# Optimization experiments

Hardware: AMD Instinct MI355X
Metric: run time of the kernel (lower is better)

Reference implementation:

```python
import jax, jax.numpy as jnp
import numpy as np

C = 128
K = 7
RED = 4
C_RED = C // RED
PAD = (K - 1) // 2
BN_EPS = 1e-5


def setup_inputs() -> dict:
    key = jax.random.key(0)
    ks = jax.random.split(key, 7)
    b, h, w = 8, 56, 56
    x = jax.random.normal(ks[0], (b, C, h, w), dtype=jnp.float32)
    # 1x1 conv #1: c -> c_red
    w1 = jax.random.normal(ks[1], (C_RED, C), dtype=jnp.float32) * (1.0 / np.sqrt(C))
    b1 = jax.random.normal(ks[2], (C_RED,), dtype=jnp.float32) * 0.01
    # BatchNorm affine params
    gamma = jnp.ones((C_RED,), dtype=jnp.float32)
    beta = jnp.zeros((C_RED,), dtype=jnp.float32)
    # 1x1 conv #2: c_red -> k*k
    w2 = jax.random.normal(ks[3], (K * K, C_RED), dtype=jnp.float32) * (1.0 / np.sqrt(C_RED))
    b2 = jax.random.normal(ks[4], (K * K,), dtype=jnp.float32) * 0.01
    return {"x": x, "w1": w1, "b1": b1, "gamma": gamma, "beta": beta, "w2": w2, "b2": b2}


def _unfold(x):
    # torch.nn.Unfold(K, padding=PAD, stride=1) -> (b, c, k*k, h, w), channel-major
    b, c, h, w = x.shape
    xp = jnp.pad(x, ((0, 0), (0, 0), (PAD, PAD), (PAD, PAD)))
    patches = [xp[:, :, i:i + h, j:j + w] for i in range(K) for j in range(K)]
    return jnp.stack(patches, axis=2)  # (b, c, k*k, h, w)


def reference(x, w1, b1, gamma, beta, w2, b2):
    b, c, h, w = x.shape
    # kernel-generation branch: 1x1 conv -> BN (batch stats, training mode) -> ReLU -> 1x1 conv
    t = jnp.einsum('rc,bchw->brhw', w1, x) + b1[None, :, None, None]
    mean = t.mean(axis=(0, 2, 3))
    var = t.var(axis=(0, 2, 3))  # biased, as in torch BN normalization
    t = (t - mean[None, :, None, None]) * jax.lax.rsqrt(var + BN_EPS)[None, :, None, None]
    t = jax.nn.relu(t * gamma[None, :, None, None] + beta[None, :, None, None])
    kern = jnp.einsum('kr,brhw->bkhw', w2, t) + b2[None, :, None, None]  # (b, k*k, h, w)
    # involution: per-pixel kernel broadcast over channels, sum over k*k taps
    x_unf = _unfold(x)  # (b, c, k*k, h, w)
    return jnp.einsum('bkhw,bckhw->bchw', kern, x_unf)
```

## Files before the change

### kernel.cpp

```cpp
#include <hip/hip_runtime.h>

#define C 128
#define CRED 32
#define K 7
#define KK 49
#define H 56
#define W 56
#define P (H*W)
#define B 8
#define NPIX (B*P)
#define BN_EPS 1e-5

#define T_OFF 0
#define T_SIZE (B*CRED*P)
#define KERN_OFF (T_OFF + T_SIZE)
#define KERN_SIZE (B*KK*P)
#define NBLK_A (49*B)
#define PSUM_OFF (KERN_OFF + KERN_SIZE)
#define PSQ_OFF (PSUM_OFF + NBLK_A*CRED)
#define SS_OFF  (PSQ_OFF + NBLK_A*CRED)
#define SCALE_OFF SS_OFF
#define SHIFT_OFF (SS_OFF + CRED)
#define WS_NEED ((size_t)(SHIFT_OFF + CRED) * sizeof(float))

#define FB_SCALE_OFF T_SIZE
#define FB_SHIFT_OFF (T_SIZE + CRED)

__global__ __launch_bounds__(256) void kA_conv1(const float* __restrict__ x,
                                                const float* __restrict__ w1,
                                                const float* __restrict__ b1,
                                                float* __restrict__ ws) {
    int tid = threadIdx.x;
    int bx = blockIdx.x;
    int b  = blockIdx.y;
    int px = tid & 63;
    int p  = bx * 64 + px;
    int ru8 = __builtin_amdgcn_readfirstlane((tid >> 6) * 8);
    const float* __restrict__ wq = w1 + (size_t)ru8 * C;
    const float* xb = x + (size_t)b * C * P + p;

    float acc[8];
#pragma unroll
    for (int u = 0; u < 8; ++u) acc[u] = 0.f;
#pragma unroll 8
    for (int c = 0; c < C; ++c) {
        float xv = xb[(size_t)c * P];
#pragma unroll
        for (int u = 0; u < 8; ++u)
            acc[u] = fmaf(wq[u * C + c], xv, acc[u]);
    }
#pragma unroll
    for (int u = 0; u < 8; ++u) acc[u] += b1[ru8 + u];

    float* tb = ws + T_OFF + (size_t)b * CRED * P + p;
#pragma unroll
    for (int u = 0; u < 8; ++u)
        tb[(size_t)(ru8 + u) * P] = acc[u];

    float s[8], q[8];
#pragma unroll
    for (int u = 0; u < 8; ++u) { s[u] = acc[u]; q[u] = acc[u] * acc[u]; }
#pragma unroll
    for (int off = 32; off; off >>= 1) {
#pragma unroll
        for (int u = 0; u < 8; ++u) {
            s[u] += __shfl_xor(s[u], off);
            q[u] += __shfl_xor(q[u], off);
        }
    }
    if (px == 0) {
        int blk = b * 49 + bx;
        float* psum = ws + PSUM_OFF + (size_t)blk * CRED + ru8;
        float* psq  = ws + PSQ_OFF  + (size_t)blk * CRED + ru8;
#pragma unroll
        for (int u = 0; u < 8; ++u) { psum[u] = s[u]; psq[u] = q[u]; }
    }
}

__global__ __launch_bounds__(256) void kCB_kern(const float* __restrict__ w2,
                                                const float* __restrict__ b2,
                                                const float* __restrict__ gamma,
                                                const float* __restrict__ beta,
                                                float* __restrict__ ws) {
    __shared__ float s_t[CRED * W];
    __shared__ float s_w2[KK * 33];
    __shared__ double sd1[8][CRED];
    __shared__ double sd2[8][CRED];
    __shared__ float s_sc[CRED];
    __shared__ float s_sh[CRED];
    int tid = threadIdx.x;
    int h = blockIdx.x, b = blockIdx.y;

    {
        int r = tid & 31, seg = tid >> 5;
        double s1 = 0.0, s2 = 0.0;
        for (int i = seg * 49; i < seg * 49 + 49; ++i) {
            s1 += (double)ws[PSUM_OFF + i * CRED + r];
            s2 += (double)ws[PSQ_OFF + i * CRED + r];
        }
        sd1[seg][r] = s1; sd2[seg][r] = s2;
    }
    for (int i = tid; i < KK * CRED; i += 256) {
        int k = i >> 5, r = i & 31;
        s_w2[k * 33 + r] = w2[i];
    }
    for (int i = tid; i < CRED * W; i += 256) {
        int r = i / W, w = i - r * W;
        s_t[i] = ws[T_OFF + ((size_t)b * CRED + r) * P + h * W + w];
    }
    __syncthreads();
    if (tid < CRED) {
        double S1 = 0.0, S2 = 0.0;
        for (int g = 0; g < 8; ++g) { S1 += sd1[g][tid]; S2 += sd2[g][tid]; }
        double mean = S1 / NPIX;
        double var = S2 / NPIX - mean * mean;
        double sc = (double)gamma[tid] / sqrt(var + BN_EPS);
        s_sc[tid] = (float)sc;
        s_sh[tid] = (float)((double)beta[tid] - mean * sc);
    }
    __syncthreads();
    for (int i = tid; i < CRED * W; i += 256) {
        int r = i / W;
        s_t[i] = fmaxf(fmaf(s_t[i], s_sc[r], s_sh[r]), 0.f);
    }
    __syncthreads();
    for (int i = tid; i < KK * 14; i += 256) {
        int k = i / 14, w0 = (i - k * 14) * 4;
        float bb = b2[k];
        float a0 = bb, a1 = bb, a2 = bb, a3 = bb;
#pragma unroll
        for (int r = 0; r < CRED; ++r) {
            float4 tv = *(const float4*)&s_t[r * W + w0];
            float wv = s_w2[k * 33 + r];
            a0 = fmaf(wv, tv.x, a0);
            a1 = fmaf(wv, tv.y, a1);
            a2 = fmaf(wv, tv.z, a2);
            a3 = fmaf(wv, tv.w, a3);
        }
        float4 o = {a0, a1, a2, a3};
        *(float4*)&ws[KERN_OFF + ((size_t)b * KK + k) * P + h * W + w0] = o;
    }
}

#define TH 7
#define XROWS 13
#define XPITCH 68
__global__ __launch_bounds__(448) void kD_inv(const float* __restrict__ x,
                                              const float* __restrict__ ws,
                                              float* __restrict__ out) {
    __shared__ float4 s_x[2][XROWS * XPITCH];
    int tid = threadIdx.x;
    int bx = blockIdx.x;
    int z  = blockIdx.y;
    int b = bx >> 3, ht = bx & 7;
    int h0 = ht * TH;
    int orow = tid / W;
    int ocol = tid - orow * W;
    int sbase = orow * XPITCH + ocol;
    bool owns = orow < TH;

    int q0 = tid, q1 = tid + 448;
    int row0 = q0 >> 6, col0 = q0 & 63;
    int hh0 = h0 - 3 + row0, ww0 = col0 - 3;
    float m0 = ((unsigned)hh0 < H && (unsigned)ww0 < W) ? 1.f : 0.f;
    int off0 = (m0 != 0.f) ? (hh0 * W + ww0) : 0;
    int slot0 = row0 * XPITCH + col0;
    int row1 = q1 >> 6, col1 = q1 & 63;
    int hh1 = h0 - 3 + row1, ww1 = col1 - 3;
    bool in1 = q1 < XROWS * 64;
    float m1 = (in1 && (unsigned)hh1 < H && (unsigned)ww1 < W) ? 1.f : 0.f;
    int off1 = (m1 != 0.f) ? (hh1 * W + ww1) : 0;
    int slot1 = row1 * XPITCH + col1;

    int cg0 = z * 16;
    const size_t xbase = ((size_t)b * C + cg0) * P;

    const float* xc0 = x + xbase;
    float4 f0, f1;
    f0.x = xc0[off0] * m0;          f0.y = xc0[P + off0] * m0;
    f0.z = xc0[2 * P + off0] * m0;  f0.w = xc0[3 * P + off0] * m0;
    f1.x = xc0[off1] * m1;          f1.y = xc0[P + off1] * m1;
    f1.z = xc0[2 * P + off1] * m1;  f1.w = xc0[3 * P + off1] * m1;

    float kr[KK];
    {
        int kidx = h0 * W + tid;
        if (kidx > P - 1) kidx = P - 1;
        const float* kb = ws + KERN_OFF + (size_t)b * KK * P + kidx;
#pragma unroll
        for (int k = 0; k < KK; ++k) kr[k] = kb[(size_t)k * P];
    }

    s_x[0][slot0] = f0;
    if (in1) s_x[0][slot1] = f1;

    for (int it = 0; it < 4; ++it) {
        __syncthreads();
        float4 n0, n1;
        if (it < 3) {
            const float* xc = x + xbase + (size_t)(it + 1) * 4 * P;
            n0.x = xc[off0] * m0;          n0.y = xc[P + off0] * m0;
            n0.z = xc[2 * P + off0] * m0;  n0.w = xc[3 * P + off0] * m0;
            n1.x = xc[off1] * m1;          n1.y = xc[P + off1] * m1;
            n1.z = xc[2 * P + off1] * m1;  n1.w = xc[3 * P + off1] * m1;
        }
        if (owns) {
            const float4* xs = s_x[it & 1] + sbase;
            float a0 = 0.f, a1 = 0.f, a2 = 0.f, a3 = 0.f;
#pragma unroll
            for (int i = 0; i < K; ++i) {
#pragma unroll
                for (int j = 0; j < K; ++j) {
                    float4 xv = xs[i * XPITCH + j];
                    float kv = kr[i * 7 + j];
                    a0 = fmaf(kv, xv.x, a0);
                    a1 = fmaf(kv, xv.y, a1);
                    a2 = fmaf(kv, xv.z, a2);
                    a3 = fmaf(kv, xv.w, a3);
                }
            }
            float* ob = out + xbase + (size_t)it * 4 * P + (size_t)h0 * W + tid;
            ob[0]     = a0;
            ob[P]     = a1;
            ob[2 * P] = a2;
            ob[3 * P] = a3;
        }
        if (it < 3) {
            float4* nb = s_x[(it + 1) & 1];
            nb[slot0] = n0;
            if (in1) nb[slot1] = n1;
        }
    }
}

__global__ __launch_bounds__(256) void k1_conv1(const float* __restrict__ x,
                                                const float* __restrict__ w1,
                                                const float* __restrict__ b1,
                                                float* __restrict__ t) {
    __shared__ float s_w1t[C * CRED];
    int tid = threadIdx.x;
    for (int i = tid; i < C * CRED; i += 256) {
        int c = i >> 5, r = i & 31;
        s_w1t[i] = w1[r * C + c];
    }
    __syncthreads();
    int b = blockIdx.y;
    int p = blockIdx.x * 256 + tid;
    if (p >= P) return;
    float acc[CRED];
#pragma unroll
    for (int r = 0; r < CRED; ++r) acc[r] = 0.f;
    const float* xb = x + (size_t)b * C * P + p;
    for (int c = 0; c < C; ++c) {
        float xv = xb[(size_t)c * P];
#pragma unroll
        for (int r = 0; r < CRED; ++r)
            acc[r] = fmaf(s_w1t[c * CRED + r], xv, acc[r]);
    }
    float* tb = t + (size_t)b * CRED * P + p;
#pragma unroll
    for (int r = 0; r < CRED; ++r)
        tb[(size_t)r * P] = acc[r] + b1[r];
}

__global__ __launch_bounds__(256) void k2_bnstats(const float* __restrict__ t,
                                                  const float* __restrict__ gamma,
                                                  const float* __restrict__ beta,
                                                  float* __restrict__ scale,
                                                  float* __restrict__ shift) {
    int r = blockIdx.x;
    int tid = threadIdx.x;
    double s = 0.0, s2 = 0.0;
    for (int i = tid; i < NPIX; i += 256) {
        int b = i / P, p = i - b * P;
        float v = t[((size_t)b * CRED + r) * P + p];
        s += v;
        s2 += (double)v * v;
    }
    __shared__ double ls[256], ls2[256];
    ls[tid] = s; ls2[tid] = s2;
    __syncthreads();
    for (int off = 128; off > 0; off >>= 1) {
        if (tid < off) { ls[tid] += ls[tid + off]; ls2[tid] += ls2[tid + off]; }
        __syncthreads();
    }
    if (tid == 0) {
        double mean = ls[0] / NPIX;
        double var = ls2[0] / NPIX - mean * mean;
        double sc = (double)gamma[r] / sqrt(var + BN_EPS);
        scale[r] = (float)sc;
        shift[r] = (float)((double)beta[r] - mean * sc);
    }
}

__global__ __launch_bounds__(256) void k3_involution(const float* __restrict__ x,
                                                     const float* __restrict__ t,
                                                     const float* __restrict__ scale,
                                                     const float* __restrict__ shift,
                                                     const float* __restrict__ w2,
                                                     const float* __restrict__ b2,
                                                     float* __restrict__ out) {
    int h = blockIdx.x;
    int b = blockIdx.y;
    int z = blockIdx.z;
    int tid = threadIdx.x;
    __shared__ float s_w2[KK * CRED];
    __shared__ float s_t[CRED * W];
    __shared__ float s_kern[KK][W];
    __shared__ float s_x[4][K][64];
    for (int i = tid; i < KK * CRED; i += 256) s_w2[i] = w2[i];
    for (int i = tid; i < CRED * W; i += 256) {
        int r = i / W, w = i - r * W;
        float v = t[((size_t)b * CRED + r) * P + h * W + w];
        v = fmaf(v, scale[r], shift[r]);
        s_t[r * W + w] = fmaxf(v, 0.f);
    }
    __syncthreads();
    for (int i = tid; i < KK * W; i += 256) {
        int k = i / W, w = i - k * W;
        float acc = b2[k];
#pragma unroll
        for (int r = 0; r < CRED; ++r)
            acc = fmaf(s_w2[k * CRED + r], s_t[r * W + w], acc);
        s_kern[k][w] = acc;
    }
    __syncthreads();
    int w = tid % W;
    int c4 = tid / W;
    float kr[KK];
#pragma unroll
    for (int k = 0; k < KK; ++k) kr[k] = s_kern[k][w];
    int cbase = z * (C / 2);
    for (int cg = cbase; cg < cbase + C / 2; cg += 4) {
        for (int i = tid; i < 4 * K * 64; i += 256) {
            int col = i & 63;
            int rc = i >> 6;
            int cc = rc / K;
            int row = rc - cc * K;
            int hh = h - 3 + row;
            int ww = col - 3;
            float v = 0.f;
            if ((unsigned)hh < H && (unsigned)ww < W)
                v = x[(((size_t)b * C + cg + cc) * H + hh) * W + ww];
            s_x[cc][row][col] = v;
        }
        __syncthreads();
        if (tid < 4 * W) {
            float acc = 0.f;
#pragma unroll
            for (int i = 0; i < K; ++i)
#pragma unroll
                for (int j = 0; j < K; ++j)
                    acc = fmaf(kr[i * K + j], s_x[c4][i][w + j], acc);
            out[(((size_t)b * C + cg + c4) * H + h) * W + w] = acc;
        }
        __syncthreads();
    }
}

extern "C" void kernel_launch(void* const* d_in, const int* in_sizes, int n_in,
                              void* d_out, int out_size, void* d_ws, size_t ws_size,
                              hipStream_t stream) {
    const float* x     = (const float*)d_in[0];
    const float* w1    = (const float*)d_in[1];
    const float* b1    = (const float*)d_in[2];
    const float* gamma = (const float*)d_in[3];
    const float* beta  = (const float*)d_in[4];
    const float* w2    = (const float*)d_in[5];
    const float* b2    = (const float*)d_in[6];
    float* out = (float*)d_out;
    float* ws  = (float*)d_ws;

    if (ws_size >= WS_NEED) {
        dim3 gA(49, B);
        kA_conv1<<<gA, 256, 0, stream>>>(x, w1, b1, ws);
        dim3 gC(H, B);
        kCB_kern<<<gC, 256, 0, stream>>>(w2, b2, gamma, beta, ws);
        dim3 gD(64, 8);
        kD_inv<<<gD, 448, 0, stream>>>(x, ws, out);
    } else {
        float* t     = ws;
        float* scale = ws + FB_SCALE_OFF;
        float* shift = ws + FB_SHIFT_OFF;
        dim3 g1((P + 255) / 256, B);
        k1_conv1<<<g1, 256, 0, stream>>>(x, w1, b1, t);
        k2_bnstats<<<CRED, 256, 0, stream>>>(t, gamma, beta, scale, shift);
        dim3 g3(H, B, 2);
        k3_involution<<<g3, 256, 0, stream>>>(x, t, scale, shift, w2, b2, out);
    }
}
```

Baseline: 48.46 us.

## Fuse BN-finalize and kernel-generation conv into the involution kernel

Drops the separate kernel-generation launch. The involution kernel now reduces the BN partial stats, applies BN+ReLU to its pixel's 32 reduced channels and computes the 49 taps in registers. This removes the round trip of the per-pixel kernel tensor through global memory and one launch. To pay for the recomputation, each block now covers 32 channels instead of 16, which halves the grid to 256 blocks and could hurt occupancy. The per-thread register arrays (32 + 49 floats) add register pressure.

```diff
diff --git a/kernel.cpp b/kernel.cpp
--- a/kernel.cpp
+++ b/kernel.cpp
@@ -13,15 +13,10 @@
 
 #define T_OFF 0
 #define T_SIZE (B*CRED*P)
-#define KERN_OFF (T_OFF + T_SIZE)
-#define KERN_SIZE (B*KK*P)
 #define NBLK_A (49*B)
-#define PSUM_OFF (KERN_OFF + KERN_SIZE)
+#define PSUM_OFF (T_OFF + T_SIZE)
 #define PSQ_OFF (PSUM_OFF + NBLK_A*CRED)
-#define SS_OFF  (PSQ_OFF + NBLK_A*CRED)
-#define SCALE_OFF SS_OFF
-#define SHIFT_OFF (SS_OFF + CRED)
-#define WS_NEED ((size_t)(SHIFT_OFF + CRED) * sizeof(float))
+#define WS_NEED ((size_t)(PSQ_OFF + NBLK_A*CRED) * sizeof(float))
 
 #define FB_SCALE_OFF T_SIZE
 #define FB_SHIFT_OFF (T_SIZE + CRED)
@@ -77,78 +72,22 @@
     }
 }
 
-__global__ __launch_bounds__(256) void kCB_kern(const float* __restrict__ w2,
+#define TH 7
+#define XROWS 13
+#define XPITCH 68
+__global__ __launch_bounds__(448) void kF_fused(const float* __restrict__ x,
+                                                const float* __restrict__ w2,
                                                 const float* __restrict__ b2,
                                                 const float* __restrict__ gamma,
                                                 const float* __restrict__ beta,
-                                                float* __restrict__ ws) {
-    __shared__ float s_t[CRED * W];
-    __shared__ float s_w2[KK * 33];
-    __shared__ double sd1[8][CRED];
-    __shared__ double sd2[8][CRED];
+                                                const float* __restrict__ ws,
+                                                float* __restrict__ out) {
+    __shared__ float4 s_x[2][XROWS * XPITCH];
+    __shared__ double sd1[14][CRED];
+    __shared__ double sd2[14][CRED];
     __shared__ float s_sc[CRED];
     __shared__ float s_sh[CRED];
-    int tid = threadIdx.x;
-    int h = blockIdx.x, b = blockIdx.y;
-
-    {
-        int r = tid & 31, seg = tid >> 5;
-        double s1 = 0.0, s2 = 0.0;
-        for (int i = seg * 49; i < seg * 49 + 49; ++i) {
-            s1 += (double)ws[PSUM_OFF + i * CRED + r];
-            s2 += (double)ws[PSQ_OFF + i * CRED + r];
-        }
-        sd1[seg][r] = s1; sd2[seg][r] = s2;
-    }
-    for (int i = tid; i < KK * CRED; i += 256) {
-        int k = i >> 5, r = i & 31;
-        s_w2[k * 33 + r] = w2[i];
-    }
-    for (int i = tid; i < CRED * W; i += 256) {
-        int r = i / W, w = i - r * W;
-        s_t[i] = ws[T_OFF + ((size_t)b * CRED + r) * P + h * W + w];
-    }
-    __syncthreads();
-    if (tid < CRED) {
-        double S1 = 0.0, S2 = 0.0;
-        for (int g = 0; g < 8; ++g) { S1 += sd1[g][tid]; S2 += sd2[g][tid]; }
-        double mean = S1 / NPIX;
-        double var = S2 / NPIX - mean * mean;
-        double sc = (double)gamma[tid] / sqrt(var + BN_EPS);
-        s_sc[tid] = (float)sc;
-        s_sh[tid] = (float)((double)beta[tid] - mean * sc);
-    }
-    __syncthreads();
-    for (int i = tid; i < CRED * W; i += 256) {
-        int r = i / W;
-        s_t[i] = fmaxf(fmaf(s_t[i], s_sc[r], s_sh[r]), 0.f);
-    }
-    __syncthreads();
-    for (int i = tid; i < KK * 14; i += 256) {
-        int k = i / 14, w0 = (i - k * 14) * 4;
-        float bb = b2[k];
-        float a0 = bb, a1 = bb, a2 = bb, a3 = bb;
-#pragma unroll
-        for (int r = 0; r < CRED; ++r) {
-            float4 tv = *(const float4*)&s_t[r * W + w0];
-            float wv = s_w2[k * 33 + r];
-            a0 = fmaf(wv, tv.x, a0);
-            a1 = fmaf(wv, tv.y, a1);
-            a2 = fmaf(wv, tv.z, a2);
-            a3 = fmaf(wv, tv.w, a3);
-        }
-        float4 o = {a0, a1, a2, a3};
-        *(float4*)&ws[KERN_OFF + ((size_t)b * KK + k) * P + h * W + w0] = o;
-    }
-}
-
-#define TH 7
-#define XROWS 13
-#define XPITCH 68
-__global__ __launch_bounds__(448) void kD_inv(const float* __restrict__ x,
-                                              const float* __restrict__ ws,
-                                              float* __restrict__ out) {
-    __shared__ float4 s_x[2][XROWS * XPITCH];
+
     int tid = threadIdx.x;
     int bx = blockIdx.x;
     int z  = blockIdx.y;
@@ -172,7 +111,7 @@
     int off1 = (m1 != 0.f) ? (hh1 * W + ww1) : 0;
     int slot1 = row1 * XPITCH + col1;
 
-    int cg0 = z * 16;
+    int cg0 = z * 32;
     const size_t xbase = ((size_t)b * C + cg0) * P;
 
     const float* xc0 = x + xbase;
@@ -182,22 +121,55 @@
     f1.x = xc0[off1] * m1;          f1.y = xc0[P + off1] * m1;
     f1.z = xc0[2 * P + off1] * m1;  f1.w = xc0[3 * P + off1] * m1;
 
+    {
+        int r = tid & 31, seg = tid >> 5;
+        double s1 = 0.0, s2 = 0.0;
+        for (int i = seg * 28; i < seg * 28 + 28; ++i) {
+            s1 += (double)ws[PSUM_OFF + i * CRED + r];
+            s2 += (double)ws[PSQ_OFF + i * CRED + r];
+        }
+        sd1[seg][r] = s1; sd2[seg][r] = s2;
+    }
+    __syncthreads();
+    if (tid < CRED) {
+        double S1 = 0.0, S2 = 0.0;
+#pragma unroll
+        for (int g = 0; g < 14; ++g) { S1 += sd1[g][tid]; S2 += sd2[g][tid]; }
+        double mean = S1 / NPIX;
+        double var = S2 / NPIX - mean * mean;
+        double sc = (double)gamma[tid] / sqrt(var + BN_EPS);
+        s_sc[tid] = (float)sc;
+        s_sh[tid] = (float)((double)beta[tid] - mean * sc);
+    }
+    __syncthreads();
+
     float kr[KK];
     {
-        int kidx = h0 * W + tid;
-        if (kidx > P - 1) kidx = P - 1;
-        const float* kb = ws + KERN_OFF + (size_t)b * KK * P + kidx;
-#pragma unroll
-        for (int k = 0; k < KK; ++k) kr[k] = kb[(size_t)k * P];
+        int pp = h0 * W + ((tid < 392) ? tid : 391);
+        const float* tp = ws + T_OFF + (size_t)b * CRED * P + pp;
+        float tv[CRED];
+#pragma unroll
+        for (int r = 0; r < CRED; ++r) tv[r] = tp[(size_t)r * P];
+#pragma unroll
+        for (int r = 0; r < CRED; ++r)
+            tv[r] = fmaxf(fmaf(tv[r], s_sc[r], s_sh[r]), 0.f);
+#pragma unroll
+        for (int k = 0; k < KK; ++k) {
+            float a = b2[k];
+#pragma unroll
+            for (int r = 0; r < CRED; ++r)
+                a = fmaf(w2[k * CRED + r], tv[r], a);
+            kr[k] = a;
+        }
     }
 
     s_x[0][slot0] = f0;
     if (in1) s_x[0][slot1] = f1;
 
-    for (int it = 0; it < 4; ++it) {
+    for (int it = 0; it < 8; ++it) {
         __syncthreads();
         float4 n0, n1;
-        if (it < 3) {
+        if (it < 7) {
             const float* xc = x + xbase + (size_t)(it + 1) * 4 * P;
             n0.x = xc[off0] * m0;          n0.y = xc[P + off0] * m0;
             n0.z = xc[2 * P + off0] * m0;  n0.w = xc[3 * P + off0] * m0;
@@ -225,7 +197,7 @@
             ob[2 * P] = a2;
             ob[3 * P] = a3;
         }
-        if (it < 3) {
+        if (it < 7) {
             float4* nb = s_x[(it + 1) & 1];
             nb[slot0] = n0;
             if (in1) nb[slot1] = n1;
@@ -374,10 +346,8 @@
     if (ws_size >= WS_NEED) {
         dim3 gA(49, B);
         kA_conv1<<<gA, 256, 0, stream>>>(x, w1, b1, ws);
-        dim3 gC(H, B);
-        kCB_kern<<<gC, 256, 0, stream>>>(w2, b2, gamma, beta, ws);
-        dim3 gD(64, 8);
-        kD_inv<<<gD, 448, 0, stream>>>(x, ws, out);
+        dim3 gF(64, 4);
+        kF_fused<<<gF, 448, 0, stream>>>(x, w2, b2, gamma, beta, ws, out);
     } else {
         float* t     = ws;
         float* scale = ws + FB_SCALE_OFF;
```

Measured after the change: 71.18 us. 1.47x slower.
